# Kernel optimization log

Hardware: AMD Instinct MI355X
Metric: run time of the kernel (lower is better)

## Reference

```python
import jax, jax.numpy as jnp
import numpy as np

HEADS = 8  # init kwarg
EPS = 1e-5  # torch LayerNorm default


def layer_norm(x, g, b):
    m = jnp.mean(x, axis=-1, keepdims=True)
    v = jnp.mean((x - m) ** 2, axis=-1, keepdims=True)
    return (x - m) * jax.lax.rsqrt(v + EPS) * g + b


def setup_inputs() -> dict:
    key = jax.random.key(0)
    B, N, H, DS = 16, 1024, 256, 3
    ks = jax.random.split(key, 12)
    s = 0.02
    return {
        "x_source": jax.random.normal(ks[0], (B, N, H), jnp.float32),
        "p_source": jax.random.normal(ks[1], (B, N, DS), jnp.float32),
        "x_out": jax.random.normal(ks[2], (B, N, H), jnp.float32),
        "p_out": jax.random.normal(ks[3], (B, N, DS), jnp.float32),
        # LayerNorm params (norm_conv_source / norm_conv_out)
        "g_s": jnp.ones((H,), jnp.float32),
        "b_s": jnp.zeros((H,), jnp.float32),
        "g_o": jnp.ones((H,), jnp.float32),
        "b_o": jnp.zeros((H,), jnp.float32),
        # CovariantAttention params: QKV act on the [.., 2H] concat
        "Wq": jax.random.normal(ks[4], (2 * H, H), jnp.float32) * s,
        "Wk": jax.random.normal(ks[5], (2 * H, H), jnp.float32) * s,
        "Wv": jax.random.normal(ks[6], (2 * H, H), jnp.float32) * s,
        "Wo": jax.random.normal(ks[7], (H, H), jnp.float32) * s,
        # position head (update_p=True, d_space=3)
        "Wp": jax.random.normal(ks[8], (H, DS), jnp.float32) * s,
    }


def reference(x_source, p_source, x_out, p_out, g_s, b_s, g_o, b_o, Wq, Wk, Wv, Wo, Wp):
    B, N, H = x_out.shape
    dh = H // HEADS
    # dual LayerNorm + concat
    xs = layer_norm(x_source, g_s, b_s)
    xo = layer_norm(x_out, g_o, b_o)
    f = jnp.concatenate([xs, xo], axis=-1)  # [B, N, 2H]
    # covariant cross-attention (reconstructed CovariantAttention)
    q = (f @ Wq).reshape(B, N, HEADS, dh)
    k = (f @ Wk).reshape(B, N, HEADS, dh)
    v = (f @ Wv).reshape(B, N, HEADS, dh)
    scores = jnp.einsum("bqhd,bkhd->bhqk", q, k) / jnp.sqrt(jnp.asarray(dh, f.dtype))
    alpha = jax.nn.softmax(scores, axis=-1)  # [B, heads, N, N]
    msg = jnp.einsum("bhqk,bkhd->bqhd", alpha, v).reshape(B, N, H)
    m_x_out = msg @ Wo
    # residual feature update + position head (update_p=True)
    x_out_new = x_out + m_x_out
    p_out_new = m_x_out @ Wp
    return (x_out_new, p_out_new)
```

## Files before the change

### kernel.cpp

```cpp
#include <hip/hip_runtime.h>
#include <hip/hip_bf16.h>

#define B_ 16
#define N_ 1024
#define H_ 256
#define HEADS_ 8
#define DH_ 32
#define BN_ (B_*N_)
#define F_ (2*H_)
#define QKV_ 768

typedef __attribute__((ext_vector_type(8))) __bf16 bf16x8;
typedef __attribute__((ext_vector_type(4))) float floatx4;

#define QSC 0.25506910542339896f

#if __has_builtin(__builtin_amdgcn_exp2f)
#define EXP2(x) __builtin_amdgcn_exp2f(x)
#else
#define EXP2(x) exp2f(x)
#endif

__device__ __forceinline__ unsigned short f2bf(float f) {
    union { float f; unsigned int u; } c; c.f = f;
    unsigned int u = c.u;
    return (unsigned short)((u + 0x7fffu + ((u >> 16) & 1u)) >> 16);
}
__device__ __forceinline__ float bf2f(unsigned short s) {
    union { unsigned int u; float f; } c; c.u = ((unsigned int)s) << 16;
    return c.f;
}
__device__ __forceinline__ unsigned int fbits(float f) {
    union { float f; unsigned int u; } c; c.f = f; return c.u;
}
__device__ __forceinline__ unsigned int pk2(float lo, float hi) {
    return __builtin_amdgcn_perm(fbits(hi) + 0x8000u, fbits(lo) + 0x8000u, 0x07060302u);
}

__device__ __forceinline__ void async16(const void* g, void* l) {
    __builtin_amdgcn_global_load_lds(
        (const __attribute__((address_space(1))) unsigned int*)g,
        (__attribute__((address_space(3))) unsigned int*)l,
        16, 0, 0);
}

__global__ __launch_bounds__(64) void ln_kernel(
        const float* __restrict__ xs_g, const float* __restrict__ xo_g,
        const float* __restrict__ gs, const float* __restrict__ bs,
        const float* __restrict__ go, const float* __restrict__ bo,
        unsigned short* __restrict__ f) {
    int row = blockIdx.x;
    int t = threadIdx.x;
    const float4 vs = ((const float4*)(xs_g + (size_t)row * H_))[t];
    const float4 vo = ((const float4*)(xo_g + (size_t)row * H_))[t];
    float s1 = vs.x + vs.y + vs.z + vs.w;
    float s2 = vs.x*vs.x + vs.y*vs.y + vs.z*vs.z + vs.w*vs.w;
    float o1 = vo.x + vo.y + vo.z + vo.w;
    float o2 = vo.x*vo.x + vo.y*vo.y + vo.z*vo.z + vo.w*vo.w;
    #pragma unroll
    for (int m = 1; m < 64; m <<= 1) {
        s1 += __shfl_xor(s1, m); s2 += __shfl_xor(s2, m);
        o1 += __shfl_xor(o1, m); o2 += __shfl_xor(o2, m);
    }
    const float inv = 1.0f / 256.0f;
    float ms = s1 * inv, vvs = s2 * inv - ms * ms;
    float mo = o1 * inv, vvo = o2 * inv - mo * mo;
    float rs = rsqrtf(vvs + 1e-5f);
    float ro = rsqrtf(vvo + 1e-5f);
    float4 g4s = ((const float4*)gs)[t];
    float4 b4s = ((const float4*)bs)[t];
    float4 g4o = ((const float4*)go)[t];
    float4 b4o = ((const float4*)bo)[t];
    ushort4 os, oo;
    os.x = f2bf((vs.x - ms) * rs * g4s.x + b4s.x);
    os.y = f2bf((vs.y - ms) * rs * g4s.y + b4s.y);
    os.z = f2bf((vs.z - ms) * rs * g4s.z + b4s.z);
    os.w = f2bf((vs.w - ms) * rs * g4s.w + b4s.w);
    oo.x = f2bf((vo.x - mo) * ro * g4o.x + b4o.x);
    oo.y = f2bf((vo.y - mo) * ro * g4o.y + b4o.y);
    oo.z = f2bf((vo.z - mo) * ro * g4o.z + b4o.z);
    oo.w = f2bf((vo.w - mo) * ro * g4o.w + b4o.w);
    *(ushort4*)(f + (size_t)row * F_ + 4 * t) = os;
    *(ushort4*)(f + (size_t)row * F_ + H_ + 4 * t) = oo;
}

__global__ __launch_bounds__(256) void pack_w(
        const float* __restrict__ Wq, const float* __restrict__ Wk,
        const float* __restrict__ Wv, const float* __restrict__ Wo,
        const float* __restrict__ Wp,
        unsigned short* __restrict__ WcT, unsigned short* __restrict__ WoT,
        float* __restrict__ WoP) {
    int i = blockIdx.x * 256 + threadIdx.x;
    const int total1 = QKV_ * F_;
    if (i < total1) {
        int n = i / F_, k = i % F_;
        float w;
        if (n < 256)      w = Wq[(size_t)k * H_ + n];
        else if (n < 512) w = Wk[(size_t)k * H_ + (n - 256)];
        else              w = Wv[(size_t)k * H_ + (n - 512)];
        WcT[i] = f2bf(w);
    }
    const int total2 = H_ * H_;
    if (i < total2) {
        int n = i / H_, k = i % H_;
        WoT[i] = f2bf(Wo[(size_t)k * H_ + n]);
    }
    if (i < H_ * 3) {
        int c = i / 3, j = i % 3;
        float s = 0.f;
        for (int n = 0; n < H_; ++n) s += Wo[(size_t)c * H_ + n] * Wp[n * 3 + j];
        WoP[i] = s;
    }
}

__global__ __launch_bounds__(256) void qkv_gemm(
        const unsigned short* __restrict__ f,
        const unsigned short* __restrict__ WcT,
        unsigned short* __restrict__ qb,
        unsigned short* __restrict__ kb,
        unsigned short* __restrict__ vT) {
    __shared__ __align__(16) unsigned short As[128 * 32];
    __shared__ __align__(16) unsigned short Bs[128 * 32];
    int t = threadIdx.x;
    int w = t >> 6, lane = t & 63;
    int r = lane & 15, qd = lane >> 4;
    int wm = (w >> 1) * 64, wn = (w & 1) * 64;
    int m0 = blockIdx.y * 128, n0 = blockIdx.x * 128;
    int lrow = lane >> 2, lcol = (lane & 3) * 8;
    floatx4 acc[4][4] = {};
    const unsigned short* gA = f   + (size_t)(m0 + w * 32 + lrow) * F_ + lcol;
    const unsigned short* gB = WcT + (size_t)(n0 + w * 32 + lrow) * F_ + lcol;
    unsigned short* lA = As + (w * 32) * 32;
    unsigned short* lB = Bs + (w * 32) * 32;
    for (int k0 = 0; k0 < F_; k0 += 32) {
        async16(gA + k0,            lA);
        async16(gA + k0 + 16 * F_,  lA + 16 * 32);
        async16(gB + k0,            lB);
        async16(gB + k0 + 16 * F_,  lB + 16 * 32);
        __syncthreads();
        bf16x8 aF[4], bF[4];
        #pragma unroll
        for (int mt = 0; mt < 4; ++mt)
            aF[mt] = *(const bf16x8*)(As + (wm + mt * 16 + r) * 32 + qd * 8);
        #pragma unroll
        for (int nt = 0; nt < 4; ++nt)
            bF[nt] = *(const bf16x8*)(Bs + (wn + nt * 16 + r) * 32 + qd * 8);
        #pragma unroll
        for (int mt = 0; mt < 4; ++mt)
            #pragma unroll
            for (int nt = 0; nt < 4; ++nt)
                acc[mt][nt] = __builtin_amdgcn_mfma_f32_16x16x32_bf16(aF[mt], bF[nt], acc[mt][nt], 0, 0, 0);
        __syncthreads();
    }
    #pragma unroll
    for (int nt = 0; nt < 4; ++nt) {
        int cg = n0 + wn + nt * 16 + r;
        int sec = cg >> 8;
        int hh = (cg >> 5) & 7;
        int d = cg & 31;
        #pragma unroll
        for (int mt = 0; mt < 4; ++mt) {
            int tok = m0 + wm + mt * 16 + qd * 4;
            int b = tok >> 10, tl = tok & 1023;
            size_t hb = (size_t)b * 8 + hh;
            if (sec == 0) {
                unsigned short* p = qb + (hb * 1024 + tl) * 32 + d;
                #pragma unroll
                for (int i = 0; i < 4; ++i) p[i * 32] = f2bf(acc[mt][nt][i] * QSC);
            } else if (sec == 1) {
                unsigned short* p = kb + (hb * 1024 + tl) * 32 + d;
                #pragma unroll
                for (int i = 0; i < 4; ++i) p[i * 32] = f2bf(acc[mt][nt][i]);
            } else {
                ushort4 v4;
                v4.x = f2bf(acc[mt][nt][0]); v4.y = f2bf(acc[mt][nt][1]);
                v4.z = f2bf(acc[mt][nt][2]); v4.w = f2bf(acc[mt][nt][3]);
                *(ushort4*)(vT + (hb * 32 + d) * 1024 + tl) = v4;
            }
        }
    }
}

__global__ __launch_bounds__(256) void attn(
        const unsigned short* __restrict__ qb,
        const unsigned short* __restrict__ kb,
        const unsigned short* __restrict__ vT,
        unsigned short* __restrict__ msg) {
    __shared__ float ob[4][32][66];
    __shared__ float lb[4][64];
    int blk = blockIdx.x;
    int qt = blk & 15;
    int h  = (blk >> 4) & 7;
    int b  = blk >> 7;
    int t = threadIdx.x;
    int w = t >> 6, lane = t & 63;
    int r = lane & 15, qd = lane >> 4;
    int q0 = qt * 64;
    size_t hb = (size_t)b * 8 + h;
    const unsigned short* qs = qb + hb * (1024 * 32);
    const unsigned short* ks = kb + hb * (1024 * 32);
    const unsigned short* vs = vT + hb * (32 * 1024);
    bf16x8 qf[4];
    #pragma unroll
    for (int i = 0; i < 4; ++i)
        qf[i] = *(const bf16x8*)(qs + (size_t)(q0 + i * 16 + r) * 32 + qd * 8);
    union { unsigned int u[4]; bf16x8 v; } onesu;
    onesu.u[0] = onesu.u[1] = onesu.u[2] = onesu.u[3] = 0x3F803F80u;
    const bf16x8 onesv = onesu.v;
    floatx4 o0[4] = {}, o1[4] = {}, ol[4] = {};
    int srcA = ((qd & 1) * 2) * 16 + r;
    int srcB = srcA + 16;
    bool hiq = qd >= 2;
    int kb0 = w * 256;
    for (int kc = 0; kc < 256; kc += 32) {
        int kk = kb0 + kc;
        bf16x8 kf0 = *(const bf16x8*)(ks + (size_t)(kk + r) * 32 + qd * 8);
        bf16x8 kf1 = *(const bf16x8*)(ks + (size_t)(kk + 16 + r) * 32 + qd * 8);
        bf16x8 vf0 = *(const bf16x8*)(vs + (size_t)r * 1024 + kk + qd * 8);
        bf16x8 vf1 = *(const bf16x8*)(vs + (size_t)(16 + r) * 1024 + kk + qd * 8);
        #pragma unroll
        for (int i = 0; i < 4; ++i) {
            floatx4 z = {0.f,0.f,0.f,0.f};
            floatx4 s0 = __builtin_amdgcn_mfma_f32_16x16x32_bf16(kf0, qf[i], z, 0, 0, 0);
            floatx4 s1 = __builtin_amdgcn_mfma_f32_16x16x32_bf16(kf1, qf[i], z, 0, 0, 0);
            float e0[4], e1[4];
            #pragma unroll
            for (int j = 0; j < 4; ++j) {
                e0[j] = EXP2(s0[j]);
                e1[j] = EXP2(s1[j]);
            }
            unsigned int t00 = pk2(e0[0], e0[1]), t01 = pk2(e0[2], e0[3]);
            unsigned int t10 = pk2(e1[0], e1[1]), t11 = pk2(e1[2], e1[3]);
            unsigned int a0 = __shfl((int)t00, srcA), a1 = __shfl((int)t01, srcA);
            unsigned int b0 = __shfl((int)t00, srcB), b1 = __shfl((int)t01, srcB);
            unsigned int c0 = __shfl((int)t10, srcA), c1 = __shfl((int)t11, srcA);
            unsigned int d0 = __shfl((int)t10, srcB), d1 = __shfl((int)t11, srcB);
            union { unsigned int u[4]; bf16x8 v; } pf;
            pf.u[0] = hiq ? c0 : a0;
            pf.u[1] = hiq ? c1 : a1;
            pf.u[2] = hiq ? d0 : b0;
            pf.u[3] = hiq ? d1 : b1;
            o0[i] = __builtin_amdgcn_mfma_f32_16x16x32_bf16(vf0, pf.v, o0[i], 0, 0, 0);
            o1[i] = __builtin_amdgcn_mfma_f32_16x16x32_bf16(vf1, pf.v, o1[i], 0, 0, 0);
            ol[i] = __builtin_amdgcn_mfma_f32_16x16x32_bf16(onesv, pf.v, ol[i], 0, 0, 0);
        }
    }
    #pragma unroll
    for (int i = 0; i < 4; ++i) {
        #pragma unroll
        for (int j = 0; j < 4; ++j) {
            ob[w][qd * 4 + j][i * 16 + r]      = o0[i][j];
            ob[w][16 + qd * 4 + j][i * 16 + r] = o1[i][j];
        }
        if (qd == 0) lb[w][i * 16 + r] = ol[i][0];
    }
    __syncthreads();
    {
        int q2 = t >> 2, dg = t & 3;
        float acc8[8] = {0.f,0.f,0.f,0.f,0.f,0.f,0.f,0.f};
        float L = 0.f;
        #pragma unroll
        for (int ww = 0; ww < 4; ++ww) {
            L += lb[ww][q2];
            #pragma unroll
            for (int j = 0; j < 8; ++j)
                acc8[j] += ob[ww][dg * 8 + j][q2];
        }
        float rinv = 1.0f / L;
        uint4 pkd;
        pkd.x = pk2(acc8[0] * rinv, acc8[1] * rinv);
        pkd.y = pk2(acc8[2] * rinv, acc8[3] * rinv);
        pkd.z = pk2(acc8[4] * rinv, acc8[5] * rinv);
        pkd.w = pk2(acc8[6] * rinv, acc8[7] * rinv);
        *(uint4*)(msg + ((size_t)(b * N_ + q0 + q2)) * H_ + h * DH_ + dg * 8) = pkd;
    }
}

__global__ __launch_bounds__(256) void out_gemm(
        const unsigned short* __restrict__ msg,
        const unsigned short* __restrict__ WoT,
        const float* __restrict__ x_out,
        float* __restrict__ outx) {
    __shared__ __align__(16) unsigned short As[128 * 32];
    __shared__ __align__(16) unsigned short Bs[128 * 32];
    int t = threadIdx.x;
    int w = t >> 6, lane = t & 63;
    int r = lane & 15, qd = lane >> 4;
    int wm = (w >> 1) * 64, wn = (w & 1) * 64;
    int m0 = blockIdx.y * 128, n0 = blockIdx.x * 128;
    int lrow = lane >> 2, lcol = (lane & 3) * 8;
    floatx4 acc[4][4] = {};
    const unsigned short* gA = msg + (size_t)(m0 + w * 32 + lrow) * H_ + lcol;
    const unsigned short* gB = WoT + (size_t)(n0 + w * 32 + lrow) * H_ + lcol;
    unsigned short* lA = As + (w * 32) * 32;
    unsigned short* lB = Bs + (w * 32) * 32;
    for (int k0 = 0; k0 < H_; k0 += 32) {
        async16(gA + k0,           lA);
        async16(gA + k0 + 16 * H_, lA + 16 * 32);
        async16(gB + k0,           lB);
        async16(gB + k0 + 16 * H_, lB + 16 * 32);
        __syncthreads();
        bf16x8 aF[4], bF[4];
        #pragma unroll
        for (int mt = 0; mt < 4; ++mt)
            aF[mt] = *(const bf16x8*)(As + (wm + mt * 16 + r) * 32 + qd * 8);
        #pragma unroll
        for (int nt = 0; nt < 4; ++nt)
            bF[nt] = *(const bf16x8*)(Bs + (wn + nt * 16 + r) * 32 + qd * 8);
        #pragma unroll
        for (int mt = 0; mt < 4; ++mt)
            #pragma unroll
            for (int nt = 0; nt < 4; ++nt)
                acc[mt][nt] = __builtin_amdgcn_mfma_f32_16x16x32_bf16(aF[mt], bF[nt], acc[mt][nt], 0, 0, 0);
        __syncthreads();
    }
    #pragma unroll
    for (int nt = 0; nt < 4; ++nt) {
        int cg = n0 + wn + nt * 16 + r;
        #pragma unroll
        for (int mt = 0; mt < 4; ++mt) {
            int tok = m0 + wm + mt * 16 + qd * 4;
            #pragma unroll
            for (int i = 0; i < 4; ++i) {
                size_t idx = (size_t)(tok + i) * H_ + cg;
                outx[idx] = x_out[idx] + acc[mt][nt][i];
            }
        }
    }
}

__global__ __launch_bounds__(64) void p_kernel(
        const unsigned short* __restrict__ msg, const float* __restrict__ WoP,
        float* __restrict__ outp) {
    int row = blockIdx.x;
    int t = threadIdx.x;
    float a0 = 0.f, a1 = 0.f, a2 = 0.f;
    #pragma unroll
    for (int i = 0; i < 4; ++i) {
        int c = t + 64 * i;
        float v = bf2f(msg[(size_t)row * H_ + c]);
        a0 += v * WoP[c * 3 + 0];
        a1 += v * WoP[c * 3 + 1];
        a2 += v * WoP[c * 3 + 2];
    }
    #pragma unroll
    for (int m = 1; m < 64; m <<= 1) {
        a0 += __shfl_xor(a0, m); a1 += __shfl_xor(a1, m); a2 += __shfl_xor(a2, m);
    }
    if (t == 0) {
        outp[(size_t)row * 3 + 0] = a0;
        outp[(size_t)row * 3 + 1] = a1;
        outp[(size_t)row * 3 + 2] = a2;
    }
}

extern "C" void kernel_launch(void* const* d_in, const int* in_sizes, int n_in,
                              void* d_out, int out_size, void* d_ws, size_t ws_size,
                              hipStream_t stream) {
    const float* x_source = (const float*)d_in[0];
    const float* x_out = (const float*)d_in[2];
    const float* g_s = (const float*)d_in[4];
    const float* b_s = (const float*)d_in[5];
    const float* g_o = (const float*)d_in[6];
    const float* b_o = (const float*)d_in[7];
    const float* Wq = (const float*)d_in[8];
    const float* Wk = (const float*)d_in[9];
    const float* Wv = (const float*)d_in[10];
    const float* Wo = (const float*)d_in[11];
    const float* Wp = (const float*)d_in[12];

    float* outx = (float*)d_out;
    float* outp = outx + (size_t)BN_ * H_;

    char* ws = (char*)d_ws;
    unsigned short* f_buf = (unsigned short*)(ws);
    unsigned short* WcT   = (unsigned short*)(ws + 16777216);
    unsigned short* WoT   = (unsigned short*)(ws + 17563648);
    float*          WoP   = (float*)         (ws + 17694720);
    unsigned short* qb    = (unsigned short*)(ws + 17697792);
    unsigned short* kb    = (unsigned short*)(ws + 26086400);
    unsigned short* vT    = (unsigned short*)(ws + 34475008);
    unsigned short* msg   = (unsigned short*)(ws + 42863616);

    ln_kernel<<<BN_, 64, 0, stream>>>(x_source, x_out, g_s, b_s, g_o, b_o, f_buf);
    pack_w<<<(QKV_ * F_ + 255) / 256, 256, 0, stream>>>(Wq, Wk, Wv, Wo, Wp, WcT, WoT, WoP);
    {
        dim3 g(QKV_ / 128, BN_ / 128);
        qkv_gemm<<<g, 256, 0, stream>>>(f_buf, WcT, qb, kb, vT);
    }
    attn<<<B_ * HEADS_ * (N_ / 64), 256, 0, stream>>>(qb, kb, vT, msg);
    {
        dim3 g(H_ / 128, BN_ / 128);
        out_gemm<<<g, 256, 0, stream>>>(msg, WoT, x_out, outx);
    }
    p_kernel<<<BN_, 64, 0, stream>>>(msg, WoP, outp);
}
```

Before: 200.9 us.

## Merge LayerNorm and weight packing into one launch; pack attention partials as bf16

The LayerNorm kernel and the weight packing kernel become a single launch that splits blocks by index. The LayerNorm part now handles four rows per 256-thread block instead of one row per 64-thread block. Separately, the attention cross-wave reduction stores partial outputs in shared memory as packed bf16 pairs instead of fp32, which halves LDS traffic and footprint. The bf16 storage adds rounding to the partial sums before they are combined.

```diff
diff --git a/kernel.cpp b/kernel.cpp
--- a/kernel.cpp
+++ b/kernel.cpp
@@ -44,72 +44,72 @@
         16, 0, 0);
 }
 
-__global__ __launch_bounds__(64) void ln_kernel(
+__global__ __launch_bounds__(256) void prep(
         const float* __restrict__ xs_g, const float* __restrict__ xo_g,
         const float* __restrict__ gs, const float* __restrict__ bs,
         const float* __restrict__ go, const float* __restrict__ bo,
-        unsigned short* __restrict__ f) {
-    int row = blockIdx.x;
-    int t = threadIdx.x;
-    const float4 vs = ((const float4*)(xs_g + (size_t)row * H_))[t];
-    const float4 vo = ((const float4*)(xo_g + (size_t)row * H_))[t];
-    float s1 = vs.x + vs.y + vs.z + vs.w;
-    float s2 = vs.x*vs.x + vs.y*vs.y + vs.z*vs.z + vs.w*vs.w;
-    float o1 = vo.x + vo.y + vo.z + vo.w;
-    float o2 = vo.x*vo.x + vo.y*vo.y + vo.z*vo.z + vo.w*vo.w;
-    #pragma unroll
-    for (int m = 1; m < 64; m <<= 1) {
-        s1 += __shfl_xor(s1, m); s2 += __shfl_xor(s2, m);
-        o1 += __shfl_xor(o1, m); o2 += __shfl_xor(o2, m);
-    }
-    const float inv = 1.0f / 256.0f;
-    float ms = s1 * inv, vvs = s2 * inv - ms * ms;
-    float mo = o1 * inv, vvo = o2 * inv - mo * mo;
-    float rs = rsqrtf(vvs + 1e-5f);
-    float ro = rsqrtf(vvo + 1e-5f);
-    float4 g4s = ((const float4*)gs)[t];
-    float4 b4s = ((const float4*)bs)[t];
-    float4 g4o = ((const float4*)go)[t];
-    float4 b4o = ((const float4*)bo)[t];
-    ushort4 os, oo;
-    os.x = f2bf((vs.x - ms) * rs * g4s.x + b4s.x);
-    os.y = f2bf((vs.y - ms) * rs * g4s.y + b4s.y);
-    os.z = f2bf((vs.z - ms) * rs * g4s.z + b4s.z);
-    os.w = f2bf((vs.w - ms) * rs * g4s.w + b4s.w);
-    oo.x = f2bf((vo.x - mo) * ro * g4o.x + b4o.x);
-    oo.y = f2bf((vo.y - mo) * ro * g4o.y + b4o.y);
-    oo.z = f2bf((vo.z - mo) * ro * g4o.z + b4o.z);
-    oo.w = f2bf((vo.w - mo) * ro * g4o.w + b4o.w);
-    *(ushort4*)(f + (size_t)row * F_ + 4 * t) = os;
-    *(ushort4*)(f + (size_t)row * F_ + H_ + 4 * t) = oo;
-}
-
-__global__ __launch_bounds__(256) void pack_w(
         const float* __restrict__ Wq, const float* __restrict__ Wk,
         const float* __restrict__ Wv, const float* __restrict__ Wo,
         const float* __restrict__ Wp,
+        unsigned short* __restrict__ f,
         unsigned short* __restrict__ WcT, unsigned short* __restrict__ WoT,
         float* __restrict__ WoP) {
-    int i = blockIdx.x * 256 + threadIdx.x;
-    const int total1 = QKV_ * F_;
-    if (i < total1) {
-        int n = i / F_, k = i % F_;
-        float w;
-        if (n < 256)      w = Wq[(size_t)k * H_ + n];
-        else if (n < 512) w = Wk[(size_t)k * H_ + (n - 256)];
-        else              w = Wv[(size_t)k * H_ + (n - 512)];
-        WcT[i] = f2bf(w);
-    }
-    const int total2 = H_ * H_;
-    if (i < total2) {
-        int n = i / H_, k = i % H_;
-        WoT[i] = f2bf(Wo[(size_t)k * H_ + n]);
-    }
-    if (i < H_ * 3) {
-        int c = i / 3, j = i % 3;
-        float s = 0.f;
-        for (int n = 0; n < H_; ++n) s += Wo[(size_t)c * H_ + n] * Wp[n * 3 + j];
-        WoP[i] = s;
+    if (blockIdx.x < 4096) {
+        int t = threadIdx.x & 63;
+        int row = blockIdx.x * 4 + (threadIdx.x >> 6);
+        const float4 vs = ((const float4*)(xs_g + (size_t)row * H_))[t];
+        const float4 vo = ((const float4*)(xo_g + (size_t)row * H_))[t];
+        float s1 = vs.x + vs.y + vs.z + vs.w;
+        float s2 = vs.x*vs.x + vs.y*vs.y + vs.z*vs.z + vs.w*vs.w;
+        float o1 = vo.x + vo.y + vo.z + vo.w;
+        float o2 = vo.x*vo.x + vo.y*vo.y + vo.z*vo.z + vo.w*vo.w;
+        #pragma unroll
+        for (int m = 1; m < 64; m <<= 1) {
+            s1 += __shfl_xor(s1, m); s2 += __shfl_xor(s2, m);
+            o1 += __shfl_xor(o1, m); o2 += __shfl_xor(o2, m);
+        }
+        const float inv = 1.0f / 256.0f;
+        float ms = s1 * inv, vvs = s2 * inv - ms * ms;
+        float mo = o1 * inv, vvo = o2 * inv - mo * mo;
+        float rs = rsqrtf(vvs + 1e-5f);
+        float ro = rsqrtf(vvo + 1e-5f);
+        float4 g4s = ((const float4*)gs)[t];
+        float4 b4s = ((const float4*)bs)[t];
+        float4 g4o = ((const float4*)go)[t];
+        float4 b4o = ((const float4*)bo)[t];
+        ushort4 os, oo;
+        os.x = f2bf((vs.x - ms) * rs * g4s.x + b4s.x);
+        os.y = f2bf((vs.y - ms) * rs * g4s.y + b4s.y);
+        os.z = f2bf((vs.z - ms) * rs * g4s.z + b4s.z);
+        os.w = f2bf((vs.w - ms) * rs * g4s.w + b4s.w);
+        oo.x = f2bf((vo.x - mo) * ro * g4o.x + b4o.x);
+        oo.y = f2bf((vo.y - mo) * ro * g4o.y + b4o.y);
+        oo.z = f2bf((vo.z - mo) * ro * g4o.z + b4o.z);
+        oo.w = f2bf((vo.w - mo) * ro * g4o.w + b4o.w);
+        *(ushort4*)(f + (size_t)row * F_ + 4 * t) = os;
+        *(ushort4*)(f + (size_t)row * F_ + H_ + 4 * t) = oo;
+    } else {
+        int i = (blockIdx.x - 4096) * 256 + threadIdx.x;
+        const int total1 = QKV_ * F_;
+        if (i < total1) {
+            int n = i / F_, k = i % F_;
+            float w;
+            if (n < 256)      w = Wq[(size_t)k * H_ + n];
+            else if (n < 512) w = Wk[(size_t)k * H_ + (n - 256)];
+            else              w = Wv[(size_t)k * H_ + (n - 512)];
+            WcT[i] = f2bf(w);
+        }
+        const int total2 = H_ * H_;
+        if (i < total2) {
+            int n = i / H_, k = i % H_;
+            WoT[i] = f2bf(Wo[(size_t)k * H_ + n]);
+        }
+        if (i < H_ * 3) {
+            int c = i / 3, j = i % 3;
+            float s = 0.f;
+            for (int n = 0; n < H_; ++n) s += Wo[(size_t)c * H_ + n] * Wp[n * 3 + j];
+            WoP[i] = s;
+        }
     }
 }
 
@@ -186,7 +186,7 @@
         const unsigned short* __restrict__ kb,
         const unsigned short* __restrict__ vT,
         unsigned short* __restrict__ msg) {
-    __shared__ float ob[4][32][66];
+    __shared__ unsigned int obu[4][16][66];
     __shared__ float lb[4][64];
     int blk = blockIdx.x;
     int qt = blk & 15;
@@ -247,11 +247,10 @@
     }
     #pragma unroll
     for (int i = 0; i < 4; ++i) {
-        #pragma unroll
-        for (int j = 0; j < 4; ++j) {
-            ob[w][qd * 4 + j][i * 16 + r]      = o0[i][j];
-            ob[w][16 + qd * 4 + j][i * 16 + r] = o1[i][j];
-        }
+        obu[w][qd * 2 + 0][i * 16 + r] = pk2(o0[i][0], o0[i][1]);
+        obu[w][qd * 2 + 1][i * 16 + r] = pk2(o0[i][2], o0[i][3]);
+        obu[w][8 + qd * 2 + 0][i * 16 + r] = pk2(o1[i][0], o1[i][1]);
+        obu[w][8 + qd * 2 + 1][i * 16 + r] = pk2(o1[i][2], o1[i][3]);
         if (qd == 0) lb[w][i * 16 + r] = ol[i][0];
     }
     __syncthreads();
@@ -263,8 +262,13 @@
         for (int ww = 0; ww < 4; ++ww) {
             L += lb[ww][q2];
             #pragma unroll
-            for (int j = 0; j < 8; ++j)
-                acc8[j] += ob[ww][dg * 8 + j][q2];
+            for (int jj = 0; jj < 4; ++jj) {
+                unsigned int u = obu[ww][dg * 4 + jj][q2];
+                union { unsigned int u; float f; } lo, hi;
+                lo.u = u << 16; hi.u = u & 0xffff0000u;
+                acc8[jj * 2]     += lo.f;
+                acc8[jj * 2 + 1] += hi.f;
+            }
         }
         float rinv = 1.0f / L;
         uint4 pkd;
@@ -382,8 +386,8 @@
     unsigned short* vT    = (unsigned short*)(ws + 34475008);
     unsigned short* msg   = (unsigned short*)(ws + 42863616);
 
-    ln_kernel<<<BN_, 64, 0, stream>>>(x_source, x_out, g_s, b_s, g_o, b_o, f_buf);
-    pack_w<<<(QKV_ * F_ + 255) / 256, 256, 0, stream>>>(Wq, Wk, Wv, Wo, Wp, WcT, WoT, WoP);
+    prep<<<4096 + 1536, 256, 0, stream>>>(x_source, x_out, g_s, b_s, g_o, b_o,
+                                          Wq, Wk, Wv, Wo, Wp, f_buf, WcT, WoT, WoP);
     {
         dim3 g(QKV_ / 128, BN_ / 128);
         qkv_gemm<<<g, 256, 0, stream>>>(f_buf, WcT, qb, kb, vT);
```

New measurement: 202.5 us. Within noise of the previous version (+0.8%).
